# Performance work log

Measured on AMD Instinct MI355X. Metric: run time of the kernel, lower is better.

Reference implementation:

```python
import jax, jax.numpy as jnp
import numpy as np
import math

NB, NS, NHID, NLAYERS, EPG = 16, 2048, 64, 4, 32768  # graphs, nodes/graph, hidden, layers, edges/graph
EPS = 1e-5


def fibonacci_sphere(n):
    i = np.arange(n, dtype=np.float64)
    phi = math.pi * (3.0 - math.sqrt(5.0))
    y = 1.0 - 2.0 * i / (n - 1)
    r = np.sqrt(np.maximum(0.0, 1.0 - y * y))
    th = phi * i
    return jnp.asarray(np.stack([np.cos(th) * r, y, np.sin(th) * r], axis=1), dtype=jnp.float32)


def _lin(k, fan_in, shape):
    b = 1.0 / float(np.sqrt(fan_in))
    return jax.random.uniform(k, shape, jnp.float32, -b, b)


def setup_inputs():
    key = jax.random.key(0)
    ks = list(jax.random.split(key, 16))
    N = NB * NS
    xyz = jax.random.normal(ks[0], (N, 3), jnp.float32)
    x = xyz / jnp.linalg.norm(xyz, axis=1, keepdims=True)  # points on unit sphere
    off = (jnp.arange(NB, dtype=jnp.int32) * NS)[:, None]
    edge_src = (jax.random.randint(ks[1], (NB, EPG), 0, NS, jnp.int32) + off).reshape(-1)
    edge_dst = (jax.random.randint(ks[2], (NB, EPG), 0, NS, jnp.int32) + off).reshape(-1)
    h = NHID
    return dict(
        x=x, edge_src=edge_src, edge_dst=edge_dst, nbatch=NB,
        enc_W=_lin(ks[3], 3, (3, h)), enc_b=_lin(ks[4], 3, (h,)),
        m1_W=_lin(ks[5], 2 * h, (NLAYERS, 2 * h, h)), m1_b=_lin(ks[6], 2 * h, (NLAYERS, h)),
        m2_W=_lin(ks[7], h, (NLAYERS, h, h)), m2_b=_lin(ks[8], h, (NLAYERS, h)),
        u1_W=_lin(ks[9], 2 * h, (NLAYERS, 2 * h, h)), u1_b=_lin(ks[10], 2 * h, (NLAYERS, h)),
        u2_W=_lin(ks[11], h, (NLAYERS, h, h)), u2_b=_lin(ks[12], h, (NLAYERS, h)),
        dec_W=_lin(ks[13], h, (h, 3)), dec_b=_lin(ks[14], h, (3,)),
    )


def _forward(x, edge_src, edge_dst, nbatch, enc_W, enc_b, m1_W, m1_b, m2_W, m2_b,
             u1_W, u1_b, u2_W, u2_b, dec_W, dec_b):
    N = x.shape[0]
    h = x @ enc_W + enc_b  # [N, nhid]

    def layer(h, p):
        m1W, m1b, m2W, m2b, u1W, u1b, u2W, u2b = p
        xi, xj = h[edge_dst], h[edge_src]                      # edge gather [E, nhid]
        m = jax.nn.relu(jnp.concatenate([xi, xj], axis=-1) @ m1W + m1b)
        m = jax.nn.relu(m @ m2W + m2b)
        agg = jax.ops.segment_sum(m, edge_dst, num_segments=N)  # scatter-add aggregate
        u = jax.nn.relu(jnp.concatenate([h, agg], axis=-1) @ u1W + u1b)
        u = jax.nn.relu(u @ u2W + u2b)
        # InstanceNorm per graph (batch is contiguous blocks), affine=False, biased var
        g = u.reshape(nbatch, -1, u.shape[-1])
        mean = g.mean(axis=1, keepdims=True)
        var = ((g - mean) ** 2).mean(axis=1, keepdims=True)
        g = (g - mean) * jax.lax.rsqrt(var + EPS)
        return g.reshape(N, -1), None

    h, _ = jax.lax.scan(layer, h, (m1_W, m1_b, m2_W, m2_b, u1_W, u1_b, u2_W, u2_b))
    X = h @ dec_W + dec_b
    X = X / jnp.linalg.norm(X, axis=-1, keepdims=True)
    X = X.reshape(nbatch, -1, 3)  # [B, nsamples, 3]

    Y = fibonacci_sphere(64)
    inv2s2 = 2.0  # 1 / (2 * sigma^2), sigma = 0.5
    kXX = jnp.exp((jnp.einsum('bnd,bmd->bnm', X, X) - 1.0) * inv2s2).mean(axis=(1, 2))
    kXY = jnp.exp((jnp.einsum('bnd,md->bnm', X, Y) - 1.0) * inv2s2).mean(axis=(1, 2))
    kYY = jnp.exp((Y @ Y.T - 1.0) * inv2s2).mean()
    loss = (kXX - 2.0 * kXY + kYY).mean()
    return loss, X


def reference(x, edge_src, edge_dst, nbatch, enc_W, enc_b, m1_W, m1_b, m2_W, m2_b,
              u1_W, u1_b, u2_W, u2_b, dec_W, dec_b):
    return _forward(x, edge_src, edge_dst, nbatch, enc_W, enc_b, m1_W, m1_b, m2_W, m2_b,
                    u1_W, u1_b, u2_W, u2_b, dec_W, dec_b)
```

## Files before the change

kernel.cpp:

```cpp
#include <hip/hip_runtime.h>
#include <cmath>

#define NNODES 32768
#define NEDGES 524288
#define NBATCH 16
#define NSAMP  2048
#define EPS    1e-5f

#define PK2 72

typedef short s16x8 __attribute__((ext_vector_type(8)));
typedef float f32x4 __attribute__((ext_vector_type(4)));
typedef unsigned short ushort_t;

struct YArr { float v[192]; };

static __device__ __forceinline__ unsigned short f2bf(float f) {
  unsigned int u = __float_as_uint(f);
  u = (u + 0x7fffu + ((u >> 16) & 1u)) >> 16;
  return (unsigned short)u;
}
static __device__ __forceinline__ float bf2f(unsigned short b) {
  return __uint_as_float(((unsigned int)b) << 16);
}

static __device__ __forceinline__ void pack2(float v0, float v1,
                                             unsigned int& ph, unsigned int& pl) {
  asm("v_cvt_pk_bf16_f32 %0, %1, %2" : "=v"(ph) : "v"(v0), "v"(v1));
  float h0 = __uint_as_float(ph << 16);
  float h1 = __uint_as_float(ph & 0xffff0000u);
  asm("v_cvt_pk_bf16_f32 %0, %1, %2" : "=v"(pl) : "v"(v0 - h0), "v"(v1 - h1));
}

__global__ __launch_bounds__(256) void setup_kernel(
    const float* __restrict__ m1W, const float* __restrict__ m2W,
    const float* __restrict__ u1W, const float* __restrict__ u2W,
    ushort_t* __restrict__ wc_hi, ushort_t* __restrict__ wc_lo,
    ushort_t* __restrict__ w1b_hi, ushort_t* __restrict__ w1b_lo,
    ushort_t* __restrict__ w2e_hi, ushort_t* __restrict__ w2e_lo,
    ushort_t* __restrict__ w2n_hi, ushort_t* __restrict__ w2n_lo,
    const int* __restrict__ edst, int* __restrict__ cnt)
{
  if (blockIdx.x >= 384) {
    int e = (blockIdx.x - 384) * 256 + threadIdx.x;
    if (e < NEDGES) atomicAdd(&cnt[edst[e]], 1);
    return;
  }
  int t = blockIdx.x * 256 + threadIdx.x;
  if (t >= 4 * 24576) return;
  int l = t / 24576;
  int r = t % 24576;
  float w; ushort_t *dh, *dl;
  if (r < 12288) {
    int j = r >> 6, k = r & 63;
    if (j < 64)       w = m1W[l*8192 + k*64 + j];
    else if (j < 128) w = m1W[l*8192 + (64 + k)*64 + (j - 64)];
    else              w = u1W[l*8192 + k*64 + (j - 128)];
    int off = l*192*PK2 + j*PK2 + k;
    dh = wc_hi + off; dl = wc_lo + off;
  } else if (r < 16384) {
    int idx = r - 12288;
    int j = idx & 63, k = idx >> 6;
    w = u1W[l*8192 + (64 + k)*64 + j];
    int off = l*64*PK2 + j*PK2 + k;
    dh = w1b_hi + off; dl = w1b_lo + off;
  } else if (r < 20480) {
    int idx = r - 16384;
    int j = idx & 63, k = idx >> 6;
    w = m2W[l*4096 + k*64 + j];
    int off = l*64*PK2 + j*PK2 + k;
    dh = w2e_hi + off; dl = w2e_lo + off;
  } else {
    int idx = r - 20480;
    int j = idx & 63, k = idx >> 6;
    w = u2W[l*4096 + k*64 + j];
    int off = l*64*PK2 + j*PK2 + k;
    dh = w2n_hi + off; dl = w2n_lo + off;
  }
  unsigned short hb = f2bf(w);
  *dh = hb;
  *dl = f2bf(w - bf2f(hb));
}

__global__ __launch_bounds__(1024) void scan_kernel(const int* __restrict__ cnt,
                                                    int* __restrict__ offs,
                                                    int* __restrict__ cursor) {
  __shared__ int sc[1024];
  int tid = threadIdx.x;
  int base = tid * 32;
  int s = 0;
  #pragma unroll
  for (int i = 0; i < 32; i++) s += cnt[base + i];
  sc[tid] = s; __syncthreads();
  int own = s;
  for (int off = 1; off < 1024; off <<= 1) {
    int v = (tid >= off) ? sc[tid - off] : 0;
    __syncthreads();
    sc[tid] += v;
    __syncthreads();
  }
  int run = sc[tid] - own;
  for (int i = 0; i < 32; i++) {
    offs[base + i] = run; cursor[base + i] = run;
    run += cnt[base + i];
  }
}

__global__ __launch_bounds__(256) void fill_kernel(
    const int* __restrict__ esrc, const int* __restrict__ edst,
    int* __restrict__ cursor, int* __restrict__ psrc, int* __restrict__ pdst) {
  int e = blockIdx.x * 256 + threadIdx.x;
  if (e < NEDGES) {
    int d = edst[e];
    int pos = atomicAdd(&cursor[d], 1);
    psrc[pos] = esrc[e];
    pdst[pos] = d;
  }
}

template<int MODE>
__global__ __launch_bounds__(256) void norm_pqr_kernel(
    const float* __restrict__ in,
    const float* __restrict__ sA, const float* __restrict__ sB,
    const float* __restrict__ encW, const float* __restrict__ encb,
    const ushort_t* __restrict__ Wh, const ushort_t* __restrict__ Wl,
    float* __restrict__ P, float* __restrict__ Q, float* __restrict__ Rb)
{
  __shared__ __align__(16) ushort_t sAh[4][16*PK2];
  __shared__ __align__(16) ushort_t sAl[4][16*PK2];
  int tid = threadIdx.x, lane = tid & 63, wave = tid >> 6;
  int l15 = lane & 15, quad = lane >> 4;
  int base = blockIdx.x * 64 + wave * 16;
  int g = blockIdx.x >> 5;

  float mean = 0.f, rstd = 1.f, w0 = 0.f, w1 = 0.f, w2 = 0.f, bb = 0.f;
  if (MODE) {
    float a = sA[g*64 + lane], q = sB[g*64 + lane];
    mean = a * (1.f / NSAMP);
    float var = q * (1.f / NSAMP) - mean * mean;
    rstd = rsqrtf(var + EPS);
  } else {
    w0 = encW[lane]; w1 = encW[64 + lane]; w2 = encW[128 + lane];
    bb = encb[lane];
  }

  ushort_t* ah_s = sAh[wave];
  ushort_t* al_s = sAl[wave];
  #pragma unroll
  for (int r = 0; r < 16; r += 2) {
    int n = base + r;
    float v0, v1;
    if (MODE) {
      v0 = (in[(size_t)n*64 + lane] - mean) * rstd;
      v1 = (in[(size_t)(n+1)*64 + lane] - mean) * rstd;
    } else {
      v0 = fmaf(in[n*3+2], w2, fmaf(in[n*3+1], w1, fmaf(in[n*3+0], w0, bb)));
      v1 = fmaf(in[(n+1)*3+2], w2, fmaf(in[(n+1)*3+1], w1, fmaf(in[(n+1)*3+0], w0, bb)));
    }
    unsigned int ph, pl;
    pack2(v0, v1, ph, pl);
    ah_s[r*PK2 + lane]     = (ushort_t)(ph & 0xffffu);
    ah_s[(r+1)*PK2 + lane] = (ushort_t)(ph >> 16);
    al_s[r*PK2 + lane]     = (ushort_t)(pl & 0xffffu);
    al_s[(r+1)*PK2 + lane] = (ushort_t)(pl >> 16);
  }

  s16x8 ah[2], al[2];
  #pragma unroll
  for (int kb = 0; kb < 2; kb++) {
    int idx = l15*PK2 + kb*32 + quad*8;
    ah[kb] = *(const s16x8*)&ah_s[idx];
    al[kb] = *(const s16x8*)&al_s[idx];
  }

  #pragma unroll
  for (int ct = 0; ct < 12; ct++) {
    f32x4 acc = (f32x4){0.f, 0.f, 0.f, 0.f};
    #pragma unroll
    for (int kb = 0; kb < 2; kb++) {
      int woff = (ct*16 + l15)*PK2 + kb*32 + quad*8;
      s16x8 bh = *(const s16x8*)(Wh + woff);
      s16x8 bl = *(const s16x8*)(Wl + woff);
      acc = __builtin_amdgcn_mfma_f32_16x16x32_bf16(al[kb], bh, acc, 0, 0, 0);
      acc = __builtin_amdgcn_mfma_f32_16x16x32_bf16(ah[kb], bl, acc, 0, 0, 0);
      acc = __builtin_amdgcn_mfma_f32_16x16x32_bf16(ah[kb], bh, acc, 0, 0, 0);
    }
    int j = ct*16 + l15;
    float* dst; int jj;
    if (ct < 4)      { dst = P;  jj = j; }
    else if (ct < 8) { dst = Q;  jj = j - 64; }
    else             { dst = Rb; jj = j - 128; }
    #pragma unroll
    for (int rr = 0; rr < 4; rr++) {
      int row = base + quad*4 + rr;
      dst[(size_t)row*64 + jj] = acc[rr];
    }
  }
}

__global__ __launch_bounds__(256, 3) void edge_fused_kernel(
    const float* __restrict__ Pbuf, const float* __restrict__ Qbuf,
    const int* __restrict__ psrc, const int* __restrict__ pdst,
    const float* __restrict__ b1,
    const ushort_t* __restrict__ W2hi, const ushort_t* __restrict__ W2lo,
    const float* __restrict__ b2,
    float* __restrict__ agg)
{
  __shared__ __align__(16) char smem[4][9216];
  __shared__ int  sSDb[2][4][64];

  int tid = threadIdx.x;
  int lane = tid & 63, wave = tid >> 6;
  int l15 = lane & 15, quad = lane >> 4;

  ushort_t* mh = (ushort_t*)smem[wave];
  ushort_t* ml = mh + 32*PK2;
  float*    m2 = (float*)smem[wave];

  s16x8 w2h[2][4], w2l[2][4];
  #pragma unroll
  for (int kb = 0; kb < 2; kb++)
    #pragma unroll
    for (int ct = 0; ct < 4; ct++) {
      int off = (ct*16 + l15)*PK2 + kb*32 + quad*8;
      w2h[kb][ct] = *(const s16x8*)(W2hi + off);
      w2l[kb][ct] = *(const s16x8*)(W2lo + off);
    }
  float b1v = b1[lane];
  float b2v[4];
  #pragma unroll
  for (int ct = 0; ct < 4; ct++) b2v[ct] = b2[ct*16 + l15];

  const int* tb = (lane < 32) ? psrc : pdst;
  int lidx = lane & 31;
  int step = gridDim.x * 128;
  int base0 = blockIdx.x * 128;

  int sidx = tb[base0 + wave*32 + lidx];
  sSDb[0][wave][lane] = sidx;

  float pv[2][8], qv[2][8];
  #pragma unroll
  for (int i = 0; i < 8; i++) {
    int s = sSDb[0][wave][i];
    int d = sSDb[0][wave][32 + i];
    qv[0][i] = Qbuf[((size_t)s << 6) + lane];
    pv[0][i] = Pbuf[((size_t)d << 6) + lane];
  }

  int cb = 0;
  for (int base = base0; base < NEDGES; base += step) {
    const int* sc = sSDb[cb][wave];
    int nb = base + step;
    int havenext = nb < NEDGES;
    if (havenext) sidx = tb[nb + wave*32 + lidx];

    #pragma unroll
    for (int rb = 0; rb < 4; rb++) {
      int cur = rb & 1;
      if (rb < 3) {
        #pragma unroll
        for (int i = 0; i < 8; i++) {
          int r = (rb+1)*8 + i;
          qv[cur^1][i] = Qbuf[((size_t)sc[r] << 6) + lane];
          pv[cur^1][i] = Pbuf[((size_t)sc[32 + r] << 6) + lane];
        }
      }
      #pragma unroll
      for (int i = 0; i < 8; i += 2) {
        int r = rb*8 + i;
        float v0 = fmaxf(pv[cur][i]   + qv[cur][i]   + b1v, 0.f);
        float v1 = fmaxf(pv[cur][i+1] + qv[cur][i+1] + b1v, 0.f);
        unsigned int ph, pl;
        pack2(v0, v1, ph, pl);
        mh[r*PK2 + lane]     = (ushort_t)(ph & 0xffffu);
        mh[(r+1)*PK2 + lane] = (ushort_t)(ph >> 16);
        ml[r*PK2 + lane]     = (ushort_t)(pl & 0xffffu);
        ml[(r+1)*PK2 + lane] = (ushort_t)(pl >> 16);
      }
    }

    f32x4 facc[2][4];
    #pragma unroll
    for (int rt = 0; rt < 2; rt++)
      #pragma unroll
      for (int ct = 0; ct < 4; ct++)
        facc[rt][ct] = (f32x4){0.f, 0.f, 0.f, 0.f};

    #pragma unroll
    for (int kb = 0; kb < 2; kb++) {
      s16x8 mhf[2], mlf[2];
      #pragma unroll
      for (int rt = 0; rt < 2; rt++) {
        int idx = (rt*16 + l15)*PK2 + kb*32 + quad*8;
        mhf[rt] = *(const s16x8*)&mh[idx];
        mlf[rt] = *(const s16x8*)&ml[idx];
      }
      #pragma unroll
      for (int ct = 0; ct < 4; ct++)
        #pragma unroll
        for (int rt = 0; rt < 2; rt++) {
          facc[rt][ct] = __builtin_amdgcn_mfma_f32_16x16x32_bf16(mlf[rt], w2h[kb][ct], facc[rt][ct], 0, 0, 0);
          facc[rt][ct] = __builtin_amdgcn_mfma_f32_16x16x32_bf16(mhf[rt], w2l[kb][ct], facc[rt][ct], 0, 0, 0);
          facc[rt][ct] = __builtin_amdgcn_mfma_f32_16x16x32_bf16(mhf[rt], w2h[kb][ct], facc[rt][ct], 0, 0, 0);
        }
    }

    if (havenext) {
      int* sn = sSDb[cb ^ 1][wave];
      sn[lane] = sidx;
      #pragma unroll
      for (int i = 0; i < 8; i++) {
        qv[0][i] = Qbuf[((size_t)sn[i] << 6) + lane];
        pv[0][i] = Pbuf[((size_t)sn[32 + i] << 6) + lane];
      }
    }

    #pragma unroll
    for (int rt = 0; rt < 2; rt++)
      #pragma unroll
      for (int ct = 0; ct < 4; ct++)
        #pragma unroll
        for (int r = 0; r < 4; r++)
          m2[(rt*16 + quad*4 + r)*68 + ct*16 + l15] = fmaxf(facc[rt][ct][r] + b2v[ct], 0.f);

    int curd = sc[32];
    float acc = 0.f;
    #pragma unroll
    for (int r = 0; r < 32; r++) {
      int d = sc[32 + r];
      float v = m2[r*68 + lane];
      if (d != curd) {
        unsafeAtomicAdd(&agg[((size_t)curd << 6) + lane], acc);
        acc = 0.f; curd = d;
      }
      acc += v;
    }
    unsafeAtomicAdd(&agg[((size_t)curd << 6) + lane], acc);

    cb ^= 1;
  }
}

__global__ __launch_bounds__(256) void node_mfma_kernel(
    const float* __restrict__ aggF, const float* __restrict__ Rbuf,
    const ushort_t* __restrict__ W1h, const ushort_t* __restrict__ W1l,
    const float* __restrict__ b1,
    const ushort_t* __restrict__ W2h, const ushort_t* __restrict__ W2l,
    const float* __restrict__ b2,
    float* __restrict__ uout, float* __restrict__ sA, float* __restrict__ sB)
{
  __shared__ __align__(16) ushort_t sMh[4][16*PK2];
  __shared__ __align__(16) ushort_t sMl[4][16*PK2];
  int tid = threadIdx.x, lane = tid & 63, wave = tid >> 6;
  int l15 = lane & 15, quad = lane >> 4;
  int base = blockIdx.x * 64 + wave * 16;
  int g = blockIdx.x >> 5;

  s16x8 ah[2], al[2];
  {
    int em = base + l15;
    #pragma unroll
    for (int kb = 0; kb < 2; kb++) {
      size_t off = (size_t)em*64 + kb*32 + quad*8;
      float4 v0 = *(const float4*)(aggF + off);
      float4 v1 = *(const float4*)(aggF + off + 4);
      float vv[8] = {v0.x,v0.y,v0.z,v0.w,v1.x,v1.y,v1.z,v1.w};
      s16x8 hh, ll;
      #pragma unroll
      for (int j = 0; j < 8; j += 2) {
        unsigned int ph, pl;
        pack2(vv[j], vv[j+1], ph, pl);
        hh[j]   = (short)(ph & 0xffffu);
        hh[j+1] = (short)(ph >> 16);
        ll[j]   = (short)(pl & 0xffffu);
        ll[j+1] = (short)(pl >> 16);
      }
      ah[kb] = hh; al[kb] = ll;
    }
  }

  ushort_t* mh = sMh[wave];
  ushort_t* ml = sMl[wave];
  float b1v[4], b2v[4];
  #pragma unroll
  for (int ct = 0; ct < 4; ct++) { b1v[ct] = b1[ct*16+l15]; b2v[ct] = b2[ct*16+l15]; }

  #pragma unroll
  for (int ct = 0; ct < 4; ct++) {
    f32x4 acc = (f32x4){0.f, 0.f, 0.f, 0.f};
    #pragma unroll
    for (int kb = 0; kb < 2; kb++) {
      int woff = (ct*16 + l15)*PK2 + kb*32 + quad*8;
      s16x8 bh = *(const s16x8*)(W1h + woff);
      s16x8 bl = *(const s16x8*)(W1l + woff);
      acc = __builtin_amdgcn_mfma_f32_16x16x32_bf16(al[kb], bh, acc, 0, 0, 0);
      acc = __builtin_amdgcn_mfma_f32_16x16x32_bf16(ah[kb], bl, acc, 0, 0, 0);
      acc = __builtin_amdgcn_mfma_f32_16x16x32_bf16(ah[kb], bh, acc, 0, 0, 0);
    }
    int j = ct*16 + l15;
    #pragma unroll
    for (int rr = 0; rr < 4; rr += 2) {
      int row = quad*4 + rr;
      float v0 = fmaxf(acc[rr]   + Rbuf[(size_t)(base+row)*64   + j] + b1v[ct], 0.f);
      float v1 = fmaxf(acc[rr+1] + Rbuf[(size_t)(base+row+1)*64 + j] + b1v[ct], 0.f);
      unsigned int ph, pl;
      pack2(v0, v1, ph, pl);
      mh[row*PK2 + j]     = (ushort_t)(ph & 0xffffu);
      mh[(row+1)*PK2 + j] = (ushort_t)(ph >> 16);
      ml[row*PK2 + j]     = (ushort_t)(pl & 0xffffu);
      ml[(row+1)*PK2 + j] = (ushort_t)(pl >> 16);
    }
  }

  s16x8 mhf[2], mlf[2];
  #pragma unroll
  for (int kb = 0; kb < 2; kb++) {
    int idx = l15*PK2 + kb*32 + quad*8;
    mhf[kb] = *(const s16x8*)&mh[idx];
    mlf[kb] = *(const s16x8*)&ml[idx];
  }
  #pragma unroll
  for (int ct = 0; ct < 4; ct++) {
    f32x4 facc = (f32x4){0.f, 0.f, 0.f, 0.f};
    #pragma unroll
    for (int kb = 0; kb < 2; kb++) {
      int woff = (ct*16 + l15)*PK2 + kb*32 + quad*8;
      s16x8 bh = *(const s16x8*)(W2h + woff);
      s16x8 bl = *(const s16x8*)(W2l + woff);
      facc = __builtin_amdgcn_mfma_f32_16x16x32_bf16(mlf[kb], bh, facc, 0, 0, 0);
      facc = __builtin_amdgcn_mfma_f32_16x16x32_bf16(mhf[kb], bl, facc, 0, 0, 0);
      facc = __builtin_amdgcn_mfma_f32_16x16x32_bf16(mhf[kb], bh, facc, 0, 0, 0);
    }
    int j = ct*16 + l15;
    float s = 0.f, s2 = 0.f;
    #pragma unroll
    for (int rr = 0; rr < 4; rr++) {
      int row = quad*4 + rr;
      float v = fmaxf(facc[rr] + b2v[ct], 0.f);
      uout[(size_t)(base+row)*64 + j] = v;
      s += v; s2 += v*v;
    }
    s  += __shfl_xor(s, 16);  s  += __shfl_xor(s, 32);
    s2 += __shfl_xor(s2, 16); s2 += __shfl_xor(s2, 32);
    if (quad == 0) {
      unsafeAtomicAdd(&sA[g*64 + j], s);
      unsafeAtomicAdd(&sB[g*64 + j], s2);
    }
  }
}

__global__ __launch_bounds__(64) void decoder_kernel(
    const float* __restrict__ u, const float* __restrict__ sA,
    const float* __restrict__ sB, const float* __restrict__ W,
    const float* __restrict__ b, float* __restrict__ X)
{
  __shared__ float sh[64][65];
  __shared__ float sm[64], sr[64];
  int lane = threadIdx.x;
  int nb = blockIdx.x * 64;
  int g = blockIdx.x >> 5;
  {
    float a = sA[g*64 + lane], q = sB[g*64 + lane];
    float mean = a * (1.f / NSAMP);
    float var = q * (1.f / NSAMP) - mean * mean;
    sm[lane] = mean;
    sr[lane] = rsqrtf(var + EPS);
  }
  for (int r = 0; r < 64; r++) sh[r][lane] = u[(size_t)(nb + r) * 64 + lane];
  __syncthreads();
  float a0 = b[0], a1 = b[1], a2 = b[2];
  #pragma unroll
  for (int c = 0; c < 64; c++) {
    float v = (sh[lane][c] - sm[c]) * sr[c];
    a0 = fmaf(v, W[c*3+0], a0);
    a1 = fmaf(v, W[c*3+1], a1);
    a2 = fmaf(v, W[c*3+2], a2);
  }
  float inv = 1.f / sqrtf(a0*a0 + a1*a1 + a2*a2);
  int n = nb + lane;
  X[n*3+0] = a0 * inv;
  X[n*3+1] = a1 * inv;
  X[n*3+2] = a2 * inv;
}

__device__ inline float block_reduce_sum(float v) {
  #pragma unroll
  for (int o = 32; o > 0; o >>= 1) v += __shfl_down(v, o, 64);
  __shared__ float red[4];
  int lane = threadIdx.x & 63, w = threadIdx.x >> 6;
  if (lane == 0) red[w] = v;
  __syncthreads();
  float t = 0.f;
  if (threadIdx.x == 0) t = red[0] + red[1] + red[2] + red[3];
  return t;
}

__global__ __launch_bounds__(256) void mmd_kernel(
    const float* __restrict__ X, YArr Y,
    float* __restrict__ kxx, float* __restrict__ kxy)
{
  if (blockIdx.x < 512) {
    int b  = blockIdx.x >> 5;
    int nt = blockIdx.x & 31;
    const float* Xb = X + (size_t)b * NSAMP * 3;
    __shared__ float sx[192];
    if (threadIdx.x < 192) sx[threadIdx.x] = Xb[nt*192 + threadIdx.x];
    __syncthreads();
    float mx0[8], mx1[8], mx2[8], ac[8];
    #pragma unroll
    for (int k = 0; k < 8; k++) {
      int m = k*256 + threadIdx.x;
      mx0[k] = Xb[m*3+0]; mx1[k] = Xb[m*3+1]; mx2[k] = Xb[m*3+2];
      ac[k] = 0.f;
    }
    for (int n = 0; n < 64; n++) {
      float s0 = sx[n*3+0], s1 = sx[n*3+1], s2 = sx[n*3+2];
      #pragma unroll
      for (int k = 0; k < 8; k++) {
        float d = fmaf(mx2[k], s2, fmaf(mx1[k], s1, mx0[k]*s0));
        ac[k] += __expf(2.f*d - 2.f);
      }
    }
    float ps = ((ac[0]+ac[1])+(ac[2]+ac[3])) + ((ac[4]+ac[5])+(ac[6]+ac[7]));
    float t2 = block_reduce_sum(ps);
    if (threadIdx.x == 0) atomicAdd(&kxx[b], t2);
  } else {
    int t  = blockIdx.x - 512;
    int b  = t >> 2;
    int ms = t & 3;
    const float* Xb = X + (size_t)b * NSAMP * 3;
    float ps = 0.f;
    #pragma unroll
    for (int it = 0; it < 2; it++) {
      int n = ms*512 + it*256 + threadIdx.x;
      float x0 = Xb[n*3+0], x1 = Xb[n*3+1], x2 = Xb[n*3+2];
      #pragma unroll
      for (int m = 0; m < 64; m++) {
        float d = x0*Y.v[m*3+0] + x1*Y.v[m*3+1] + x2*Y.v[m*3+2];
        ps += __expf(2.f*d - 2.f);
      }
    }
    float t2 = block_reduce_sum(ps);
    if (threadIdx.x == 0) atomicAdd(&kxy[b], t2);
  }
}

__global__ void loss_kernel(const float* __restrict__ kxx,
                            const float* __restrict__ kxy,
                            float kyy, float* __restrict__ out)
{
  if (threadIdx.x == 0 && blockIdx.x == 0) {
    float s = 0.f;
    for (int b = 0; b < NBATCH; b++)
      s += kxx[b] * (1.0f/((float)NSAMP*(float)NSAMP))
         - 2.0f * kxy[b] * (1.0f/((float)NSAMP*64.0f));
    out[0] = s * (1.0f/NBATCH) + kyy;
  }
}

extern "C" void kernel_launch(void* const* d_in, const int* in_sizes, int n_in,
                              void* d_out, int out_size, void* d_ws, size_t ws_size,
                              hipStream_t stream)
{
  const float* x    = (const float*)d_in[0];
  const int*   esrc = (const int*)  d_in[1];
  const int*   edst = (const int*)  d_in[2];
  const float* encW = (const float*)d_in[4];
  const float* encb = (const float*)d_in[5];
  const float* m1W  = (const float*)d_in[6];
  const float* m1b  = (const float*)d_in[7];
  const float* m2W  = (const float*)d_in[8];
  const float* m2b  = (const float*)d_in[9];
  const float* u1W  = (const float*)d_in[10];
  const float* u1b  = (const float*)d_in[11];
  const float* u2W  = (const float*)d_in[12];
  const float* u2b  = (const float*)d_in[13];
  const float* decW = (const float*)d_in[14];
  const float* decb = (const float*)d_in[15];
  float* out = (float*)d_out;

  const size_t NF = (size_t)NNODES * 64;
  float* aggAll = (float*)d_ws;
  float* statsA = aggAll + 4*NF;
  float* statsB = statsA + 4096;
  float* kxx    = statsB + 4096;
  float* kxy    = kxx + 16;
  int*   icnt   = (int*)(kxy + 16);
  size_t zero_bytes = (4*NF + 4096 + 4096 + 32) * sizeof(float) + NNODES * sizeof(int);

  float* u_buf  = (float*)(icnt + NNODES);
  float* Pbuf   = u_buf + NF;
  float* Qbuf   = Pbuf + NF;
  float* Rbuf   = Qbuf + NF;
  int* ioffs    = (int*)(Rbuf + NF + 16);
  int* icur     = ioffs + NNODES;
  int* psrc     = icur + NNODES;
  int* pdst     = psrc + NEDGES;
  ushort_t* us  = (ushort_t*)(pdst + NEDGES);
  ushort_t* wc_hi  = us;  us += 4*192*PK2;
  ushort_t* wc_lo  = us;  us += 4*192*PK2;
  ushort_t* w1b_hi = us;  us += 4*64*PK2;
  ushort_t* w1b_lo = us;  us += 4*64*PK2;
  ushort_t* w2e_hi = us;  us += 4*64*PK2;
  ushort_t* w2e_lo = us;  us += 4*64*PK2;
  ushort_t* w2n_hi = us;  us += 4*64*PK2;
  ushort_t* w2n_lo = us;  us += 4*64*PK2;

  float* X = out + 1;

  hipMemsetAsync(aggAll, 0, zero_bytes, stream);

  setup_kernel<<<384 + NEDGES/256, 256, 0, stream>>>(
      m1W, m2W, u1W, u2W,
      wc_hi, wc_lo, w1b_hi, w1b_lo, w2e_hi, w2e_lo, w2n_hi, w2n_lo,
      edst, icnt);
  scan_kernel<<<1, 1024, 0, stream>>>(icnt, ioffs, icur);
  fill_kernel<<<NEDGES/256, 256, 0, stream>>>(esrc, edst, icur, psrc, pdst);

  for (int l = 0; l < 4; l++) {
    const ushort_t* wch = wc_hi + (size_t)l*192*PK2;
    const ushort_t* wcl = wc_lo + (size_t)l*192*PK2;
    if (l == 0)
      norm_pqr_kernel<0><<<512, 256, 0, stream>>>(
          x, nullptr, nullptr, encW, encb, wch, wcl, Pbuf, Qbuf, Rbuf);
    else
      norm_pqr_kernel<1><<<512, 256, 0, stream>>>(
          u_buf, statsA + (l-1)*1024, statsB + (l-1)*1024, nullptr, nullptr,
          wch, wcl, Pbuf, Qbuf, Rbuf);

    edge_fused_kernel<<<768, 256, 0, stream>>>(
        Pbuf, Qbuf, psrc, pdst, m1b + l*64,
        w2e_hi + (size_t)l*64*PK2, w2e_lo + (size_t)l*64*PK2, m2b + l*64,
        aggAll + (size_t)l*NF);

    node_mfma_kernel<<<512, 256, 0, stream>>>(
        aggAll + (size_t)l*NF, Rbuf,
        w1b_hi + (size_t)l*64*PK2, w1b_lo + (size_t)l*64*PK2, u1b + l*64,
        w2n_hi + (size_t)l*64*PK2, w2n_lo + (size_t)l*64*PK2, u2b + l*64,
        u_buf, statsA + l*1024, statsB + l*1024);
  }

  decoder_kernel<<<NNODES/64, 64, 0, stream>>>(
      u_buf, statsA + 3*1024, statsB + 3*1024, decW, decb, X);

  YArr Y;
  {
    const double pi = 3.14159265358979323846;
    double phi = pi * (3.0 - sqrt(5.0));
    for (int i = 0; i < 64; i++) {
      double y  = 1.0 - 2.0 * (double)i / 63.0;
      double r  = sqrt(fmax(0.0, 1.0 - y*y));
      double th = phi * (double)i;
      Y.v[i*3+0] = (float)(cos(th) * r);
      Y.v[i*3+1] = (float)y;
      Y.v[i*3+2] = (float)(sin(th) * r);
    }
  }
  double kyy_acc = 0.0;
  for (int i = 0; i < 64; i++)
    for (int j = 0; j < 64; j++) {
      double d = (double)Y.v[i*3+0]*Y.v[j*3+0]
               + (double)Y.v[i*3+1]*Y.v[j*3+1]
               + (double)Y.v[i*3+2]*Y.v[j*3+2];
      kyy_acc += exp(2.0*d - 2.0);
    }
  float kyy = (float)(kyy_acc / 4096.0);

  mmd_kernel<<<512 + 64, 256, 0, stream>>>(X, Y, kxx, kxy);
  loss_kernel<<<1, 64, 0, stream>>>(kxx, kxy, kyy, out);
}
```

Baseline: 415.9 us.

## Gather edge features directly into MFMA fragments and fold m1 bias into P

The edge kernel no longer gathers per-lane scalars, packs them to bf16 hi/lo and round-trips them through LDS before the second MLP matmul. Each lane now loads float4 pairs from the P and Q rows matching its MFMA A-fragment position and packs them straight into registers. The software-pipelined prefetch of the next batch is removed. The m1 bias is added once per node when P is written, so it no longer runs per edge. This drops LDS writes and reads plus a bias add per edge, at the cost of gather latency now being exposed without explicit prefetch.

```diff
diff --git a/kernel.cpp b/kernel.cpp
--- a/kernel.cpp
+++ b/kernel.cpp
@@ -11,6 +11,7 @@
 
 typedef short s16x8 __attribute__((ext_vector_type(8)));
 typedef float f32x4 __attribute__((ext_vector_type(4)));
+typedef unsigned int u32x4 __attribute__((ext_vector_type(4)));
 typedef unsigned short ushort_t;
 
 struct YArr { float v[192]; };
@@ -124,6 +125,7 @@
     const float* __restrict__ sA, const float* __restrict__ sB,
     const float* __restrict__ encW, const float* __restrict__ encb,
     const ushort_t* __restrict__ Wh, const ushort_t* __restrict__ Wl,
+    const float* __restrict__ b1e,
     float* __restrict__ P, float* __restrict__ Q, float* __restrict__ Rb)
 {
   __shared__ __align__(16) ushort_t sAh[4][16*PK2];
@@ -186,14 +188,14 @@
       acc = __builtin_amdgcn_mfma_f32_16x16x32_bf16(ah[kb], bh, acc, 0, 0, 0);
     }
     int j = ct*16 + l15;
-    float* dst; int jj;
-    if (ct < 4)      { dst = P;  jj = j; }
+    float* dst; int jj; float addv = 0.f;
+    if (ct < 4)      { dst = P;  jj = j; addv = b1e[jj]; }
     else if (ct < 8) { dst = Q;  jj = j - 64; }
     else             { dst = Rb; jj = j - 128; }
     #pragma unroll
     for (int rr = 0; rr < 4; rr++) {
       int row = base + quad*4 + rr;
-      dst[(size_t)row*64 + jj] = acc[rr];
+      dst[(size_t)row*64 + jj] = acc[rr] + addv;
     }
   }
 }
@@ -201,21 +203,18 @@
 __global__ __launch_bounds__(256, 3) void edge_fused_kernel(
     const float* __restrict__ Pbuf, const float* __restrict__ Qbuf,
     const int* __restrict__ psrc, const int* __restrict__ pdst,
-    const float* __restrict__ b1,
     const ushort_t* __restrict__ W2hi, const ushort_t* __restrict__ W2lo,
     const float* __restrict__ b2,
     float* __restrict__ agg)
 {
-  __shared__ __align__(16) char smem[4][9216];
-  __shared__ int  sSDb[2][4][64];
+  __shared__ __align__(16) float m2s[4][32*68];
+  __shared__ int sSDb[2][4][64];
 
   int tid = threadIdx.x;
   int lane = tid & 63, wave = tid >> 6;
   int l15 = lane & 15, quad = lane >> 4;
 
-  ushort_t* mh = (ushort_t*)smem[wave];
-  ushort_t* ml = mh + 32*PK2;
-  float*    m2 = (float*)smem[wave];
+  float* m2 = m2s[wave];
 
   s16x8 w2h[2][4], w2l[2][4];
   #pragma unroll
@@ -226,7 +225,6 @@
       w2h[kb][ct] = *(const s16x8*)(W2hi + off);
       w2l[kb][ct] = *(const s16x8*)(W2lo + off);
     }
-  float b1v = b1[lane];
   float b2v[4];
   #pragma unroll
   for (int ct = 0; ct < 4; ct++) b2v[ct] = b2[ct*16 + l15];
@@ -238,15 +236,6 @@
 
   int sidx = tb[base0 + wave*32 + lidx];
   sSDb[0][wave][lane] = sidx;
-
-  float pv[2][8], qv[2][8];
-  #pragma unroll
-  for (int i = 0; i < 8; i++) {
-    int s = sSDb[0][wave][i];
-    int d = sSDb[0][wave][32 + i];
-    qv[0][i] = Qbuf[((size_t)s << 6) + lane];
-    pv[0][i] = Pbuf[((size_t)d << 6) + lane];
-  }
 
   int cb = 0;
   for (int base = base0; base < NEDGES; base += step) {
@@ -255,28 +244,40 @@
     int havenext = nb < NEDGES;
     if (havenext) sidx = tb[nb + wave*32 + lidx];
 
-    #pragma unroll
-    for (int rb = 0; rb < 4; rb++) {
-      int cur = rb & 1;
-      if (rb < 3) {
-        #pragma unroll
-        for (int i = 0; i < 8; i++) {
-          int r = (rb+1)*8 + i;
-          qv[cur^1][i] = Qbuf[((size_t)sc[r] << 6) + lane];
-          pv[cur^1][i] = Pbuf[((size_t)sc[32 + r] << 6) + lane];
-        }
+    s16x8 pah[2][2], pal[2][2];
+    #pragma unroll
+    for (int kb = 0; kb < 2; kb++) {
+      float4 qq[2][2], pp[2][2];
+      #pragma unroll
+      for (int rt = 0; rt < 2; rt++) {
+        int srow = sc[rt*16 + l15];
+        int drow = sc[32 + rt*16 + l15];
+        const float* qp = Qbuf + (((size_t)srow) << 6) + kb*32 + quad*8;
+        const float* pd = Pbuf + (((size_t)drow) << 6) + kb*32 + quad*8;
+        qq[rt][0] = *(const float4*)(qp);
+        qq[rt][1] = *(const float4*)(qp + 4);
+        pp[rt][0] = *(const float4*)(pd);
+        pp[rt][1] = *(const float4*)(pd + 4);
       }
       #pragma unroll
-      for (int i = 0; i < 8; i += 2) {
-        int r = rb*8 + i;
-        float v0 = fmaxf(pv[cur][i]   + qv[cur][i]   + b1v, 0.f);
-        float v1 = fmaxf(pv[cur][i+1] + qv[cur][i+1] + b1v, 0.f);
-        unsigned int ph, pl;
-        pack2(v0, v1, ph, pl);
-        mh[r*PK2 + lane]     = (ushort_t)(ph & 0xffffu);
-        mh[(r+1)*PK2 + lane] = (ushort_t)(ph >> 16);
-        ml[r*PK2 + lane]     = (ushort_t)(pl & 0xffffu);
-        ml[(r+1)*PK2 + lane] = (ushort_t)(pl >> 16);
+      for (int rt = 0; rt < 2; rt++) {
+        float v0 = fmaxf(pp[rt][0].x + qq[rt][0].x, 0.f);
+        float v1 = fmaxf(pp[rt][0].y + qq[rt][0].y, 0.f);
+        float v2 = fmaxf(pp[rt][0].z + qq[rt][0].z, 0.f);
+        float v3 = fmaxf(pp[rt][0].w + qq[rt][0].w, 0.f);
+        float v4 = fmaxf(pp[rt][1].x + qq[rt][1].x, 0.f);
+        float v5 = fmaxf(pp[rt][1].y + qq[rt][1].y, 0.f);
+        float v6 = fmaxf(pp[rt][1].z + qq[rt][1].z, 0.f);
+        float v7 = fmaxf(pp[rt][1].w + qq[rt][1].w, 0.f);
+        unsigned int h0,h1,h2,h3,l0,l1,l2,l3;
+        pack2(v0, v1, h0, l0);
+        pack2(v2, v3, h1, l1);
+        pack2(v4, v5, h2, l2);
+        pack2(v6, v7, h3, l3);
+        u32x4 uh = (u32x4){h0, h1, h2, h3};
+        u32x4 ul = (u32x4){l0, l1, l2, l3};
+        pah[kb][rt] = __builtin_bit_cast(s16x8, uh);
+        pal[kb][rt] = __builtin_bit_cast(s16x8, ul);
       }
     }
 
@@ -288,33 +289,17 @@
         facc[rt][ct] = (f32x4){0.f, 0.f, 0.f, 0.f};
 
     #pragma unroll
-    for (int kb = 0; kb < 2; kb++) {
-      s16x8 mhf[2], mlf[2];
-      #pragma unroll
-      for (int rt = 0; rt < 2; rt++) {
-        int idx = (rt*16 + l15)*PK2 + kb*32 + quad*8;
-        mhf[rt] = *(const s16x8*)&mh[idx];
-        mlf[rt] = *(const s16x8*)&ml[idx];
-      }
+    for (int kb = 0; kb < 2; kb++)
       #pragma unroll
       for (int ct = 0; ct < 4; ct++)
         #pragma unroll
         for (int rt = 0; rt < 2; rt++) {
-          facc[rt][ct] = __builtin_amdgcn_mfma_f32_16x16x32_bf16(mlf[rt], w2h[kb][ct], facc[rt][ct], 0, 0, 0);
-          facc[rt][ct] = __builtin_amdgcn_mfma_f32_16x16x32_bf16(mhf[rt], w2l[kb][ct], facc[rt][ct], 0, 0, 0);
-          facc[rt][ct] = __builtin_amdgcn_mfma_f32_16x16x32_bf16(mhf[rt], w2h[kb][ct], facc[rt][ct], 0, 0, 0);
+          facc[rt][ct] = __builtin_amdgcn_mfma_f32_16x16x32_bf16(pal[kb][rt], w2h[kb][ct], facc[rt][ct], 0, 0, 0);
+          facc[rt][ct] = __builtin_amdgcn_mfma_f32_16x16x32_bf16(pah[kb][rt], w2l[kb][ct], facc[rt][ct], 0, 0, 0);
+          facc[rt][ct] = __builtin_amdgcn_mfma_f32_16x16x32_bf16(pah[kb][rt], w2h[kb][ct], facc[rt][ct], 0, 0, 0);
         }
-    }
-
-    if (havenext) {
-      int* sn = sSDb[cb ^ 1][wave];
-      sn[lane] = sidx;
-      #pragma unroll
-      for (int i = 0; i < 8; i++) {
-        qv[0][i] = Qbuf[((size_t)sn[i] << 6) + lane];
-        pv[0][i] = Pbuf[((size_t)sn[32 + i] << 6) + lane];
-      }
-    }
+
+    if (havenext) sSDb[cb ^ 1][wave][lane] = sidx;
 
     #pragma unroll
     for (int rt = 0; rt < 2; rt++)
@@ -623,14 +608,15 @@
     const ushort_t* wcl = wc_lo + (size_t)l*192*PK2;
     if (l == 0)
       norm_pqr_kernel<0><<<512, 256, 0, stream>>>(
-          x, nullptr, nullptr, encW, encb, wch, wcl, Pbuf, Qbuf, Rbuf);
+          x, nullptr, nullptr, encW, encb, wch, wcl, m1b + l*64,
+          Pbuf, Qbuf, Rbuf);
     else
       norm_pqr_kernel<1><<<512, 256, 0, stream>>>(
           u_buf, statsA + (l-1)*1024, statsB + (l-1)*1024, nullptr, nullptr,
-          wch, wcl, Pbuf, Qbuf, Rbuf);
+          wch, wcl, m1b + l*64, Pbuf, Qbuf, Rbuf);
 
     edge_fused_kernel<<<768, 256, 0, stream>>>(
-        Pbuf, Qbuf, psrc, pdst, m1b + l*64,
+        Pbuf, Qbuf, psrc, pdst,
         w2e_hi + (size_t)l*64*PK2, w2e_lo + (size_t)l*64*PK2, m2b + l*64,
         aggAll + (size_t)l*NF);
 
```

New measurement: 408.2 us. Within noise of the previous version (-1.8%).
